# Performance work log

Hardware: AMD Instinct MI355X
Metric: run time of the kernel (lower is better)

The kernel has to match this reference:

```python
import jax, jax.numpy as jnp
import numpy as np

NG, NC, FG, FC, D = 8192, 4096, 512, 256, 64
ALPHA = 0.2          # leaky_relu negative slope
NEG = -9.0e15        # mask fill value from the torch code


def _leaky(x):
    return jnp.where(x >= 0, x, ALPHA * x)


def _relation(h_src, h_dst, a, adj):
    # additive GAT score: e[i,j] = leaky(h_src[i]@a[:D] + h_dst[j]@a[D:])
    s1 = h_src @ a[:D]            # [Ns]
    s2 = h_dst @ a[D:]            # [Nd]
    e = _leaky(s1[:, None] + s2[None, :])          # [Ns, Nd]
    att = jax.nn.softmax(jnp.where(adj > 0, e, NEG), axis=1)
    return att @ h_dst            # [Ns, D]


def setup_inputs() -> dict:
    key = jax.random.key(0)
    ks = jax.random.split(key, 14)
    sc = 0.05
    return {
        "gene_x": jax.random.normal(ks[0], (NG, FG), jnp.float32),
        "cell_x": jax.random.normal(ks[1], (NC, FC), jnp.float32),
        "W_g": jax.random.normal(ks[2], (FG, D), jnp.float32) * sc,
        "W_c": jax.random.normal(ks[3], (FC, D), jnp.float32) * sc,
        "a_gg": jax.random.normal(ks[4], (2 * D,), jnp.float32) * sc,
        "a_gc": jax.random.normal(ks[5], (2 * D,), jnp.float32) * sc,
        "a_cc": jax.random.normal(ks[6], (2 * D,), jnp.float32) * sc,
        "a_cg": jax.random.normal(ks[7], (2 * D,), jnp.float32) * sc,
        "Wgate_g": jax.random.normal(ks[8], (D, 1), jnp.float32) * sc,
        "bgate_g": jnp.full((1,), -2.0, jnp.float32),
        "Wgate_c": jax.random.normal(ks[9], (D, 1), jnp.float32) * sc,
        "bgate_c": jnp.full((1,), -2.0, jnp.float32),
        "gene_adj": jax.random.randint(ks[10], (NG, NG), 0, 2, jnp.int32),
        "cell_adj": jax.random.randint(ks[11], (NC, NC), 0, 2, jnp.int32),
        "gene_cell_adj": jax.random.randint(ks[12], (NG, NC), 0, 2, jnp.int32),
    }


def reference(gene_x, cell_x, W_g, W_c, a_gg, a_gc, a_cc, a_cg,
              Wgate_g, bgate_g, Wgate_c, bgate_c,
              gene_adj, cell_adj, gene_cell_adj):
    gene_h = gene_x @ W_g                              # [NG, D]
    cell_h = cell_x @ W_c                              # [NC, D]

    gene_from_gene = _relation(gene_h, gene_h, a_gg, gene_adj)
    gene_from_cell = _relation(gene_h, cell_h, a_gc, gene_cell_adj)
    cell_from_cell = _relation(cell_h, cell_h, a_cc, cell_adj)
    cell_from_gene = _relation(cell_h, gene_h, a_cg, gene_cell_adj.T)

    gamma_g = jax.nn.sigmoid(gene_h @ Wgate_g + bgate_g)   # [NG, 1]
    gamma_c = jax.nn.sigmoid(cell_h @ Wgate_c + bgate_c)   # [NC, 1]

    gene_out = _leaky(gene_h + gene_from_gene + gamma_g * gene_from_cell)
    cell_out = _leaky(cell_h + cell_from_cell + gamma_c * cell_from_gene)
    return gene_out, cell_out
```

## Files before the change

kernel.cpp:

```cpp
#include <hip/hip_runtime.h>

#define NG 8192
#define NC 4096
#define FG 512
#define FC 256
#define ALPHA 0.2f

typedef float f32x4 __attribute__((ext_vector_type(4)));
typedef short bf16x8 __attribute__((ext_vector_type(8)));

static __device__ __forceinline__ float leakyf(float x) { return fmaxf(x, ALPHA * x); }

static __device__ __forceinline__ unsigned short f2bf(float f) {
    unsigned u = __builtin_bit_cast(unsigned, f);
    u += 0x7fffu + ((u >> 16) & 1u);
    return (unsigned short)(u >> 16);
}

static __device__ __forceinline__ float wred(float v) {
#pragma unroll
    for (int m = 1; m < 64; m <<= 1) v += __shfl_xor(v, m, 64);
    return v;
}

__global__ __launch_bounds__(256) void proj_kernel(
    const float* __restrict__ x, const float* __restrict__ W, int K, int N,
    float* __restrict__ h, unsigned short* __restrict__ hT,
    const float* __restrict__ aA, const float* __restrict__ aB,
    const float* __restrict__ aC, const float* __restrict__ aD,
    const float* __restrict__ aG, const float* __restrict__ bG,
    float* __restrict__ sA, float* __restrict__ sB, float* __restrict__ sC,
    float* __restrict__ sD, float* __restrict__ gam)
{
    const int wave = threadIdx.x >> 6, lane = threadIdx.x & 63;
    const int r0 = blockIdx.x * 16 + wave * 4;
    const float* xr = x + (size_t)r0 * K;
    float acc0 = 0.f, acc1 = 0.f, acc2 = 0.f, acc3 = 0.f;
    for (int k = 0; k < K; k += 4) {
        float4 x0 = *(const float4*)(xr + k);
        float4 x1 = *(const float4*)(xr + K + k);
        float4 x2 = *(const float4*)(xr + 2 * (size_t)K + k);
        float4 x3 = *(const float4*)(xr + 3 * (size_t)K + k);
        float w0 = W[(k + 0) * 64 + lane];
        float w1 = W[(k + 1) * 64 + lane];
        float w2 = W[(k + 2) * 64 + lane];
        float w3 = W[(k + 3) * 64 + lane];
        acc0 += x0.x * w0 + x0.y * w1 + x0.z * w2 + x0.w * w3;
        acc1 += x1.x * w0 + x1.y * w1 + x1.z * w2 + x1.w * w3;
        acc2 += x2.x * w0 + x2.y * w1 + x2.z * w2 + x2.w * w3;
        acc3 += x3.x * w0 + x3.y * w1 + x3.z * w2 + x3.w * w3;
    }
    float accs[4] = {acc0, acc1, acc2, acc3};
    unsigned short hb[4];
#pragma unroll
    for (int t = 0; t < 4; t++) {
        h[(size_t)(r0 + t) * 64 + lane] = accs[t];
        hb[t] = f2bf(accs[t]);
    }
    *(ushort4*)&hT[(size_t)lane * N + r0] = make_ushort4(hb[0], hb[1], hb[2], hb[3]);

    const float cA = aA[lane], cB = aB[lane], cC = aC[lane], cD = aD[lane], cG = aG[lane];
    const float bias = bG[0];
#pragma unroll
    for (int t = 0; t < 4; t++) {
        float vA = wred(accs[t] * cA);
        float vB = wred(accs[t] * cB);
        float vC = wred(accs[t] * cC);
        float vD = wred(accs[t] * cD);
        float vG = wred(accs[t] * cG);
        if (lane == 0) {
            sA[r0 + t] = vA; sB[r0 + t] = vB; sC[r0 + t] = vC; sD[r0 + t] = vD;
            gam[r0 + t] = 1.f / (1.f + __expf(-(vG + bias)));
        }
    }
}

__global__ __launch_bounds__(256, 4) void rel_kernel(
    const int* __restrict__ adj, int adj_ld, int transposed,
    const float* __restrict__ s1, const float* __restrict__ s2,
    const unsigned short* __restrict__ hT, int Nd,
    float* __restrict__ num, float* __restrict__ lsum, int Ns, int JS)
{
    const int wave = threadIdx.x >> 6, lane = threadIdx.x & 63;
    const int m = lane & 15, kp = lane >> 4;
    const int strip = blockIdx.x, p = blockIdx.y;
    const int jlen = Nd / JS, jbase = p * jlen;
    const int i_row = strip * 64 + wave * 16 + m;
    const float s1v = s1[i_row];
    f32x4 acc0 = {0.f, 0.f, 0.f, 0.f}, acc1 = acc0, acc2 = acc0, acc3 = acc0;
    float lacc = 0.f;

    const unsigned short* hb0 = hT + (size_t)(0 * 16 + m) * Nd;
    const unsigned short* hb1 = hT + (size_t)(1 * 16 + m) * Nd;
    const unsigned short* hb2 = hT + (size_t)(2 * 16 + m) * Nd;
    const unsigned short* hb3 = hT + (size_t)(3 * 16 + m) * Nd;

    const int NGRP = jlen >> 5;
#pragma unroll 2
    for (int g = 0; g < NGRP; ++g) {
        const int jg = jbase + g * 32 + kp * 8;
        float4 sa = *(const float4*)&s2[jg];
        float4 sb = *(const float4*)&s2[jg + 4];
        int am[8];
        if (!transposed) {
            const int* ar = adj + (size_t)i_row * adj_ld + jg;
            int4 a0 = *(const int4*)ar;
            int4 a1 = *(const int4*)(ar + 4);
            am[0] = a0.x; am[1] = a0.y; am[2] = a0.z; am[3] = a0.w;
            am[4] = a1.x; am[5] = a1.y; am[6] = a1.z; am[7] = a1.w;
        } else {
            const int* ac = adj + (size_t)jg * adj_ld + i_row;
#pragma unroll
            for (int t = 0; t < 8; t++) am[t] = ac[(size_t)t * adj_ld];
        }
        bf16x8 b0 = *(const bf16x8*)&hb0[jg];
        bf16x8 b1 = *(const bf16x8*)&hb1[jg];
        bf16x8 b2 = *(const bf16x8*)&hb2[jg];
        bf16x8 b3 = *(const bf16x8*)&hb3[jg];

        float s2v[8] = {sa.x, sa.y, sa.z, sa.w, sb.x, sb.y, sb.z, sb.w};
        bf16x8 af;
#pragma unroll
        for (int t = 0; t < 8; t++) {
            float e = s1v + s2v[t];
            float w = (am[t] > 0) ? __expf(leakyf(e)) : 0.f;
            lacc += w;
            af[t] = (short)f2bf(w);
        }
        acc0 = __builtin_amdgcn_mfma_f32_16x16x32_bf16(af, b0, acc0, 0, 0, 0);
        acc1 = __builtin_amdgcn_mfma_f32_16x16x32_bf16(af, b1, acc1, 0, 0, 0);
        acc2 = __builtin_amdgcn_mfma_f32_16x16x32_bf16(af, b2, acc2, 0, 0, 0);
        acc3 = __builtin_amdgcn_mfma_f32_16x16x32_bf16(af, b3, acc3, 0, 0, 0);
    }
    const int orow0 = strip * 64 + wave * 16 + kp * 4;
#pragma unroll
    for (int r = 0; r < 4; r++) {
        size_t base = ((size_t)p * Ns + orow0 + r) * 64;
        num[base + m]      = acc0[r];
        num[base + 16 + m] = acc1[r];
        num[base + 32 + m] = acc2[r];
        num[base + 48 + m] = acc3[r];
    }
    lacc += __shfl_xor(lacc, 16, 64);
    lacc += __shfl_xor(lacc, 32, 64);
    if (kp == 0) lsum[(size_t)p * Ns + strip * 64 + wave * 16 + m] = lacc;
}

__global__ __launch_bounds__(256) void combine_final(
    const float* __restrict__ numS, const float* __restrict__ lS, int JSS,
    const float* __restrict__ numX, const float* __restrict__ lX, int JSX,
    int Ns, const float* __restrict__ h, const float* __restrict__ gam,
    float* __restrict__ out)
{
    int idx = blockIdx.x * 256 + threadIdx.x;
    int i = idx >> 6, c = idx & 63;
    float nS = 0.f, dS = 0.f, nX = 0.f, dX = 0.f;
    for (int p = 0; p < JSS; p++) {
        nS += numS[((size_t)p * Ns + i) * 64 + c];
        dS += lS[(size_t)p * Ns + i];
    }
    for (int p = 0; p < JSX; p++) {
        nX += numX[((size_t)p * Ns + i) * 64 + c];
        dX += lX[(size_t)p * Ns + i];
    }
    float v = h[idx] + nS / dS + gam[i] * (nX / dX);
    out[idx] = leakyf(v);
}

extern "C" void kernel_launch(void* const* d_in, const int* in_sizes, int n_in,
                              void* d_out, int out_size, void* d_ws, size_t ws_size,
                              hipStream_t stream)
{
    const float* gene_x = (const float*)d_in[0];
    const float* cell_x = (const float*)d_in[1];
    const float* W_g    = (const float*)d_in[2];
    const float* W_c    = (const float*)d_in[3];
    const float* a_gg   = (const float*)d_in[4];
    const float* a_gc   = (const float*)d_in[5];
    const float* a_cc   = (const float*)d_in[6];
    const float* a_cg   = (const float*)d_in[7];
    const float* Wgg    = (const float*)d_in[8];
    const float* bgg    = (const float*)d_in[9];
    const float* Wgc    = (const float*)d_in[10];
    const float* bgc    = (const float*)d_in[11];
    const int* gene_adj = (const int*)d_in[12];
    const int* cell_adj = (const int*)d_in[13];
    const int* gc_adj   = (const int*)d_in[14];

    size_t off = 0;
    char* wsb = (char*)d_ws;
    auto alloc = [&](size_t bytes) -> void* {
        void* p = wsb + off;
        off += (bytes + 255) & ~(size_t)255;
        return p;
    };
    const int JS_GG = 8, JS_CC = 16, JS_GC = 8, JS_CG = 16;

    float* gene_h = (float*)alloc((size_t)NG * 64 * 4);
    float* cell_h = (float*)alloc((size_t)NC * 64 * 4);
    unsigned short* gene_hT = (unsigned short*)alloc((size_t)NG * 64 * 2);
    unsigned short* cell_hT = (unsigned short*)alloc((size_t)NC * 64 * 2);
    float* s1gg = (float*)alloc(NG * 4);
    float* s2gg = (float*)alloc(NG * 4);
    float* s1gc = (float*)alloc(NG * 4);
    float* s2cg = (float*)alloc(NG * 4);
    float* gamg = (float*)alloc(NG * 4);
    float* s1cc = (float*)alloc(NC * 4);
    float* s2cc = (float*)alloc(NC * 4);
    float* s2gc = (float*)alloc(NC * 4);
    float* s1cg = (float*)alloc(NC * 4);
    float* gamc = (float*)alloc(NC * 4);
    float* numGG = (float*)alloc((size_t)NG * 64 * JS_GG * 4);
    float* lGG   = (float*)alloc((size_t)NG * JS_GG * 4);
    float* numGC = (float*)alloc((size_t)NG * 64 * JS_GC * 4);
    float* lGC   = (float*)alloc((size_t)NG * JS_GC * 4);
    float* numCC = (float*)alloc((size_t)NC * 64 * JS_CC * 4);
    float* lCC   = (float*)alloc((size_t)NC * JS_CC * 4);
    float* numCG = (float*)alloc((size_t)NC * 64 * JS_CG * 4);
    float* lCG   = (float*)alloc((size_t)NC * JS_CG * 4);

    float* out_gene = (float*)d_out;
    float* out_cell = (float*)d_out + (size_t)NG * 64;

    proj_kernel<<<NG / 16, 256, 0, stream>>>(gene_x, W_g, FG, NG, gene_h, gene_hT,
        a_gg, a_gg + 64, a_gc, a_cg + 64, Wgg, bgg, s1gg, s2gg, s1gc, s2cg, gamg);
    proj_kernel<<<NC / 16, 256, 0, stream>>>(cell_x, W_c, FC, NC, cell_h, cell_hT,
        a_cc, a_cc + 64, a_gc + 64, a_cg, Wgc, bgc, s1cc, s2cc, s2gc, s1cg, gamc);

    rel_kernel<<<dim3(NG / 64, JS_GG), 256, 0, stream>>>(gene_adj, NG, 0, s1gg, s2gg,
        gene_hT, NG, numGG, lGG, NG, JS_GG);
    rel_kernel<<<dim3(NC / 64, JS_CC), 256, 0, stream>>>(cell_adj, NC, 0, s1cc, s2cc,
        cell_hT, NC, numCC, lCC, NC, JS_CC);
    rel_kernel<<<dim3(NG / 64, JS_GC), 256, 0, stream>>>(gc_adj, NC, 0, s1gc, s2gc,
        cell_hT, NC, numGC, lGC, NG, JS_GC);
    rel_kernel<<<dim3(NC / 64, JS_CG), 256, 0, stream>>>(gc_adj, NC, 1, s1cg, s2cg,
        gene_hT, NG, numCG, lCG, NC, JS_CG);

    combine_final<<<NG * 64 / 256, 256, 0, stream>>>(numGG, lGG, JS_GG, numGC, lGC, JS_GC,
        NG, gene_h, gamg, out_gene);
    combine_final<<<NC * 64 / 256, 256, 0, stream>>>(numCC, lCC, JS_CC, numCG, lCG, JS_CG,
        NC, cell_h, gamc, out_cell);
}
```

Measured before the change: 763.0 us.

## Stage adjacency tiles into LDS with double-buffered async global_load_lds

Splits the relation kernel into row and column variants. Each wave stages its 16-row adjacency tile into LDS through double-buffered global_load_lds, waiting on vmcnt so the next chunk's loads overlap the current chunk's exp and MFMA work. The transposed case loads column tiles coalesced into a padded LDS layout. The J-split counts are cut, which means fewer partial sums to combine but also fewer blocks and lower occupancy, given the large LDS footprint and launch bounds of 1-2 blocks per CU.

```diff
diff --git a/kernel.cpp b/kernel.cpp
--- a/kernel.cpp
+++ b/kernel.cpp
@@ -8,6 +8,9 @@
 
 typedef float f32x4 __attribute__((ext_vector_type(4)));
 typedef short bf16x8 __attribute__((ext_vector_type(8)));
+
+#define AS1C(p) ((const __attribute__((address_space(1))) void*)(p))
+#define AS3(p)  ((__attribute__((address_space(3))) void*)(p))
 
 static __device__ __forceinline__ float leakyf(float x) { return fmaxf(x, ALPHA * x); }
 
@@ -75,62 +78,170 @@
     }
 }
 
-__global__ __launch_bounds__(256, 4) void rel_kernel(
-    const int* __restrict__ adj, int adj_ld, int transposed,
+__global__ __launch_bounds__(256, 1) void rel_row(
+    const int* __restrict__ adj, int adj_ld,
     const float* __restrict__ s1, const float* __restrict__ s2,
     const unsigned short* __restrict__ hT, int Nd,
     float* __restrict__ num, float* __restrict__ lsum, int Ns, int JS)
 {
+    __shared__ int smem[4 * 2 * 16 * 260];
     const int wave = threadIdx.x >> 6, lane = threadIdx.x & 63;
     const int m = lane & 15, kp = lane >> 4;
     const int strip = blockIdx.x, p = blockIdx.y;
     const int jlen = Nd / JS, jbase = p * jlen;
-    const int i_row = strip * 64 + wave * 16 + m;
-    const float s1v = s1[i_row];
-    f32x4 acc0 = {0.f, 0.f, 0.f, 0.f}, acc1 = acc0, acc2 = acc0, acc3 = acc0;
-    float lacc = 0.f;
+    const int i0w = strip * 64 + wave * 16;
+    const float s1v = s1[i0w + m];
+    int* wbuf = smem + wave * (2 * 16 * 260);
+    const int* arow = adj + (size_t)i0w * adj_ld + jbase;
 
     const unsigned short* hb0 = hT + (size_t)(0 * 16 + m) * Nd;
     const unsigned short* hb1 = hT + (size_t)(1 * 16 + m) * Nd;
     const unsigned short* hb2 = hT + (size_t)(2 * 16 + m) * Nd;
     const unsigned short* hb3 = hT + (size_t)(3 * 16 + m) * Nd;
 
-    const int NGRP = jlen >> 5;
-#pragma unroll 2
-    for (int g = 0; g < NGRP; ++g) {
-        const int jg = jbase + g * 32 + kp * 8;
-        float4 sa = *(const float4*)&s2[jg];
-        float4 sb = *(const float4*)&s2[jg + 4];
-        int am[8];
-        if (!transposed) {
-            const int* ar = adj + (size_t)i_row * adj_ld + jg;
-            int4 a0 = *(const int4*)ar;
-            int4 a1 = *(const int4*)(ar + 4);
-            am[0] = a0.x; am[1] = a0.y; am[2] = a0.z; am[3] = a0.w;
-            am[4] = a1.x; am[5] = a1.y; am[6] = a1.z; am[7] = a1.w;
+    f32x4 acc0 = {0.f, 0.f, 0.f, 0.f}, acc1 = acc0, acc2 = acc0, acc3 = acc0;
+    float lacc = 0.f;
+    const int NCH = jlen >> 8;
+
+    {
+        int* dst = wbuf;
+#pragma unroll
+        for (int r = 0; r < 16; ++r)
+            __builtin_amdgcn_global_load_lds(AS1C(arow + (size_t)r * adj_ld + lane * 4),
+                                             AS3(dst + r * 260), 16, 0, 0);
+    }
+    for (int c = 0; c < NCH; ++c) {
+        int* cur = wbuf + (c & 1) * (16 * 260);
+        if (c + 1 < NCH) {
+            int* dst = wbuf + ((c + 1) & 1) * (16 * 260);
+            const int* src = arow + (c + 1) * 256;
+#pragma unroll
+            for (int r = 0; r < 16; ++r)
+                __builtin_amdgcn_global_load_lds(AS1C(src + (size_t)r * adj_ld + lane * 4),
+                                                 AS3(dst + r * 260), 16, 0, 0);
+            asm volatile("s_waitcnt vmcnt(16)" ::: "memory");
         } else {
-            const int* ac = adj + (size_t)jg * adj_ld + i_row;
-#pragma unroll
-            for (int t = 0; t < 8; t++) am[t] = ac[(size_t)t * adj_ld];
-        }
-        bf16x8 b0 = *(const bf16x8*)&hb0[jg];
-        bf16x8 b1 = *(const bf16x8*)&hb1[jg];
-        bf16x8 b2 = *(const bf16x8*)&hb2[jg];
-        bf16x8 b3 = *(const bf16x8*)&hb3[jg];
-
-        float s2v[8] = {sa.x, sa.y, sa.z, sa.w, sb.x, sb.y, sb.z, sb.w};
-        bf16x8 af;
-#pragma unroll
-        for (int t = 0; t < 8; t++) {
-            float e = s1v + s2v[t];
-            float w = (am[t] > 0) ? __expf(leakyf(e)) : 0.f;
-            lacc += w;
-            af[t] = (short)f2bf(w);
-        }
-        acc0 = __builtin_amdgcn_mfma_f32_16x16x32_bf16(af, b0, acc0, 0, 0, 0);
-        acc1 = __builtin_amdgcn_mfma_f32_16x16x32_bf16(af, b1, acc1, 0, 0, 0);
-        acc2 = __builtin_amdgcn_mfma_f32_16x16x32_bf16(af, b2, acc2, 0, 0, 0);
-        acc3 = __builtin_amdgcn_mfma_f32_16x16x32_bf16(af, b3, acc3, 0, 0, 0);
+            asm volatile("s_waitcnt vmcnt(0)" ::: "memory");
+        }
+        const int jc = jbase + c * 256;
+#pragma unroll
+        for (int g = 0; g < 8; ++g) {
+            const int jg = jc + g * 32 + kp * 8;
+            float4 sa = *(const float4*)&s2[jg];
+            float4 sb = *(const float4*)&s2[jg + 4];
+            const int* ap = cur + m * 260 + g * 32 + kp * 8;
+            int4 a0 = *(const int4*)ap;
+            int4 a1 = *(const int4*)(ap + 4);
+            bf16x8 b0 = *(const bf16x8*)&hb0[jg];
+            bf16x8 b1 = *(const bf16x8*)&hb1[jg];
+            bf16x8 b2 = *(const bf16x8*)&hb2[jg];
+            bf16x8 b3 = *(const bf16x8*)&hb3[jg];
+            float s2v[8] = {sa.x, sa.y, sa.z, sa.w, sb.x, sb.y, sb.z, sb.w};
+            int am[8] = {a0.x, a0.y, a0.z, a0.w, a1.x, a1.y, a1.z, a1.w};
+            bf16x8 af;
+#pragma unroll
+            for (int t = 0; t < 8; t++) {
+                float e = s1v + s2v[t];
+                float w = (am[t] > 0) ? __expf(leakyf(e)) : 0.f;
+                lacc += w;
+                af[t] = (short)f2bf(w);
+            }
+            acc0 = __builtin_amdgcn_mfma_f32_16x16x32_bf16(af, b0, acc0, 0, 0, 0);
+            acc1 = __builtin_amdgcn_mfma_f32_16x16x32_bf16(af, b1, acc1, 0, 0, 0);
+            acc2 = __builtin_amdgcn_mfma_f32_16x16x32_bf16(af, b2, acc2, 0, 0, 0);
+            acc3 = __builtin_amdgcn_mfma_f32_16x16x32_bf16(af, b3, acc3, 0, 0, 0);
+        }
+    }
+    const int orow0 = strip * 64 + wave * 16 + kp * 4;
+#pragma unroll
+    for (int r = 0; r < 4; r++) {
+        size_t base = ((size_t)p * Ns + orow0 + r) * 64;
+        num[base + m]      = acc0[r];
+        num[base + 16 + m] = acc1[r];
+        num[base + 32 + m] = acc2[r];
+        num[base + 48 + m] = acc3[r];
+    }
+    lacc += __shfl_xor(lacc, 16, 64);
+    lacc += __shfl_xor(lacc, 32, 64);
+    if (kp == 0) lsum[(size_t)p * Ns + strip * 64 + wave * 16 + m] = lacc;
+}
+
+__global__ __launch_bounds__(256, 2) void rel_col(
+    const int* __restrict__ adj, int adj_ld,
+    const float* __restrict__ s1, const float* __restrict__ s2,
+    const unsigned short* __restrict__ hT, int Nd,
+    float* __restrict__ num, float* __restrict__ lsum, int Ns, int JS)
+{
+    __shared__ int smem[4 * 2 * 32 * 68];
+    const int wave = threadIdx.x >> 6, lane = threadIdx.x & 63;
+    const int m = lane & 15, kp = lane >> 4;
+    const int strip = blockIdx.x, p = blockIdx.y;
+    const int jlen = Nd / JS, jbase = p * jlen;
+    const int i0w = strip * 64 + wave * 16;
+    const float s1v = s1[i0w + m];
+    int* wbuf = smem + wave * (2 * 32 * 68);
+    const int lr = lane >> 4, li = lane & 15;
+
+    const unsigned short* hb0 = hT + (size_t)(0 * 16 + m) * Nd;
+    const unsigned short* hb1 = hT + (size_t)(1 * 16 + m) * Nd;
+    const unsigned short* hb2 = hT + (size_t)(2 * 16 + m) * Nd;
+    const unsigned short* hb3 = hT + (size_t)(3 * 16 + m) * Nd;
+
+    f32x4 acc0 = {0.f, 0.f, 0.f, 0.f}, acc1 = acc0, acc2 = acc0, acc3 = acc0;
+    float lacc = 0.f;
+    const int NCH = jlen >> 7;
+
+    {
+        int* dst = wbuf;
+#pragma unroll
+        for (int q = 0; q < 32; ++q)
+            __builtin_amdgcn_global_load_lds(
+                AS1C(adj + (size_t)(jbase + q * 4 + lr) * adj_ld + i0w + li),
+                AS3(dst + q * 68), 4, 0, 0);
+    }
+    for (int c = 0; c < NCH; ++c) {
+        int* cur = wbuf + (c & 1) * (32 * 68);
+        if (c + 1 < NCH) {
+            int* dst = wbuf + ((c + 1) & 1) * (32 * 68);
+            const int jn = jbase + (c + 1) * 128;
+#pragma unroll
+            for (int q = 0; q < 32; ++q)
+                __builtin_amdgcn_global_load_lds(
+                    AS1C(adj + (size_t)(jn + q * 4 + lr) * adj_ld + i0w + li),
+                    AS3(dst + q * 68), 4, 0, 0);
+            asm volatile("s_waitcnt vmcnt(32)" ::: "memory");
+        } else {
+            asm volatile("s_waitcnt vmcnt(0)" ::: "memory");
+        }
+        const int jc = jbase + c * 128;
+#pragma unroll
+        for (int g = 0; g < 4; ++g) {
+            const int jg = jc + g * 32 + kp * 8;
+            float4 sa = *(const float4*)&s2[jg];
+            float4 sb = *(const float4*)&s2[jg + 4];
+            const int* ap = cur + (g * 8 + kp * 2) * 68 + m;
+            int am[8];
+#pragma unroll
+            for (int t = 0; t < 8; t++)
+                am[t] = ap[(t >> 2) * 68 + (t & 3) * 16];
+            bf16x8 b0 = *(const bf16x8*)&hb0[jg];
+            bf16x8 b1 = *(const bf16x8*)&hb1[jg];
+            bf16x8 b2 = *(const bf16x8*)&hb2[jg];
+            bf16x8 b3 = *(const bf16x8*)&hb3[jg];
+            float s2v[8] = {sa.x, sa.y, sa.z, sa.w, sb.x, sb.y, sb.z, sb.w};
+            bf16x8 af;
+#pragma unroll
+            for (int t = 0; t < 8; t++) {
+                float e = s1v + s2v[t];
+                float w = (am[t] > 0) ? __expf(leakyf(e)) : 0.f;
+                lacc += w;
+                af[t] = (short)f2bf(w);
+            }
+            acc0 = __builtin_amdgcn_mfma_f32_16x16x32_bf16(af, b0, acc0, 0, 0, 0);
+            acc1 = __builtin_amdgcn_mfma_f32_16x16x32_bf16(af, b1, acc1, 0, 0, 0);
+            acc2 = __builtin_amdgcn_mfma_f32_16x16x32_bf16(af, b2, acc2, 0, 0, 0);
+            acc3 = __builtin_amdgcn_mfma_f32_16x16x32_bf16(af, b3, acc3, 0, 0, 0);
+        }
     }
     const int orow0 = strip * 64 + wave * 16 + kp * 4;
 #pragma unroll
@@ -194,7 +305,7 @@
         off += (bytes + 255) & ~(size_t)255;
         return p;
     };
-    const int JS_GG = 8, JS_CC = 16, JS_GC = 8, JS_CG = 16;
+    const int JS_GG = 2, JS_CC = 4, JS_GC = 2, JS_CG = 8;
 
     float* gene_h = (float*)alloc((size_t)NG * 64 * 4);
     float* cell_h = (float*)alloc((size_t)NC * 64 * 4);
@@ -227,13 +338,13 @@
     proj_kernel<<<NC / 16, 256, 0, stream>>>(cell_x, W_c, FC, NC, cell_h, cell_hT,
         a_cc, a_cc + 64, a_gc + 64, a_cg, Wgc, bgc, s1cc, s2cc, s2gc, s1cg, gamc);
 
-    rel_kernel<<<dim3(NG / 64, JS_GG), 256, 0, stream>>>(gene_adj, NG, 0, s1gg, s2gg,
+    rel_row<<<dim3(NG / 64, JS_GG), 256, 0, stream>>>(gene_adj, NG, s1gg, s2gg,
         gene_hT, NG, numGG, lGG, NG, JS_GG);
-    rel_kernel<<<dim3(NC / 64, JS_CC), 256, 0, stream>>>(cell_adj, NC, 0, s1cc, s2cc,
+    rel_row<<<dim3(NC / 64, JS_CC), 256, 0, stream>>>(cell_adj, NC, s1cc, s2cc,
         cell_hT, NC, numCC, lCC, NC, JS_CC);
-    rel_kernel<<<dim3(NG / 64, JS_GC), 256, 0, stream>>>(gc_adj, NC, 0, s1gc, s2gc,
+    rel_row<<<dim3(NG / 64, JS_GC), 256, 0, stream>>>(gc_adj, NC, s1gc, s2gc,
         cell_hT, NC, numGC, lGC, NG, JS_GC);
-    rel_kernel<<<dim3(NC / 64, JS_CG), 256, 0, stream>>>(gc_adj, NC, 1, s1cg, s2cg,
+    rel_col<<<dim3(NC / 64, JS_CG), 256, 0, stream>>>(gc_adj, NC, s1cg, s2cg,
         gene_hT, NG, numCG, lCG, NC, JS_CG);
 
     combine_final<<<NG * 64 / 256, 256, 0, stream>>>(numGG, lGG, JS_GG, numGC, lGC, JS_GC,
```

New measurement: 772.0 us. No clear change (+1.2%).

## Pack adjacency into bitmasks once and stage hT tiles in LDS

Applied to the files above, without the earlier changes.

Adds a pack_bits pass that turns each int32 adjacency matrix into a bitmask, so the four relation kernels read a compact mask rather than full ints. The shared gene-cell mask also serves the transposed relation. The relation kernel is split into row and column variants that stage hT tiles (and mask bytes for the column case) in shared memory. The split factors JS are halved. The int adjacency must still be read once in full, so the gain depends on the gene-cell matrix being reused and on cheaper transposed access, at the cost of extra launches, LDS traffic and barriers.

```diff
diff --git a/kernel.cpp b/kernel.cpp
--- a/kernel.cpp
+++ b/kernel.cpp
@@ -21,6 +21,24 @@
 #pragma unroll
     for (int m = 1; m < 64; m <<= 1) v += __shfl_xor(v, m, 64);
     return v;
+}
+
+__global__ __launch_bounds__(256) void pack_bits(
+    const int* __restrict__ adj, int C, unsigned char* __restrict__ bm)
+{
+    const int wave = threadIdx.x >> 6, lane = threadIdx.x & 63;
+    const int r = blockIdx.x * 4 + wave;
+    const int* row = adj + (size_t)r * C;
+    unsigned char* brow = bm + (size_t)r * (C >> 3);
+    for (int j = lane * 8; j < C; j += 512) {
+        int4 a0 = *(const int4*)(row + j);
+        int4 a1 = *(const int4*)(row + j + 4);
+        unsigned b = (unsigned)(a0.x > 0)        | ((unsigned)(a0.y > 0) << 1)
+                   | ((unsigned)(a0.z > 0) << 2) | ((unsigned)(a0.w > 0) << 3)
+                   | ((unsigned)(a1.x > 0) << 4) | ((unsigned)(a1.y > 0) << 5)
+                   | ((unsigned)(a1.z > 0) << 6) | ((unsigned)(a1.w > 0) << 7);
+        brow[j >> 3] = (unsigned char)b;
+    }
 }
 
 __global__ __launch_bounds__(256) void proj_kernel(
@@ -75,62 +93,128 @@
     }
 }
 
-__global__ __launch_bounds__(256, 4) void rel_kernel(
-    const int* __restrict__ adj, int adj_ld, int transposed,
+__global__ __launch_bounds__(256, 4) void rel_row(
+    const unsigned char* __restrict__ bm, int bm_ld,
     const float* __restrict__ s1, const float* __restrict__ s2,
     const unsigned short* __restrict__ hT, int Nd,
     float* __restrict__ num, float* __restrict__ lsum, int Ns, int JS)
 {
+    __shared__ unsigned short hbuf[64 * 264];
     const int wave = threadIdx.x >> 6, lane = threadIdx.x & 63;
     const int m = lane & 15, kp = lane >> 4;
     const int strip = blockIdx.x, p = blockIdx.y;
     const int jlen = Nd / JS, jbase = p * jlen;
     const int i_row = strip * 64 + wave * 16 + m;
     const float s1v = s1[i_row];
+    const unsigned char* bmrow = bm + (size_t)i_row * bm_ld;
     f32x4 acc0 = {0.f, 0.f, 0.f, 0.f}, acc1 = acc0, acc2 = acc0, acc3 = acc0;
     float lacc = 0.f;
 
-    const unsigned short* hb0 = hT + (size_t)(0 * 16 + m) * Nd;
-    const unsigned short* hb1 = hT + (size_t)(1 * 16 + m) * Nd;
-    const unsigned short* hb2 = hT + (size_t)(2 * 16 + m) * Nd;
-    const unsigned short* hb3 = hT + (size_t)(3 * 16 + m) * Nd;
-
-    const int NGRP = jlen >> 5;
-#pragma unroll 2
-    for (int g = 0; g < NGRP; ++g) {
-        const int jg = jbase + g * 32 + kp * 8;
-        float4 sa = *(const float4*)&s2[jg];
-        float4 sb = *(const float4*)&s2[jg + 4];
-        int am[8];
-        if (!transposed) {
-            const int* ar = adj + (size_t)i_row * adj_ld + jg;
-            int4 a0 = *(const int4*)ar;
-            int4 a1 = *(const int4*)(ar + 4);
-            am[0] = a0.x; am[1] = a0.y; am[2] = a0.z; am[3] = a0.w;
-            am[4] = a1.x; am[5] = a1.y; am[6] = a1.z; am[7] = a1.w;
-        } else {
-            const int* ac = adj + (size_t)jg * adj_ld + i_row;
-#pragma unroll
-            for (int t = 0; t < 8; t++) am[t] = ac[(size_t)t * adj_ld];
-        }
-        bf16x8 b0 = *(const bf16x8*)&hb0[jg];
-        bf16x8 b1 = *(const bf16x8*)&hb1[jg];
-        bf16x8 b2 = *(const bf16x8*)&hb2[jg];
-        bf16x8 b3 = *(const bf16x8*)&hb3[jg];
-
-        float s2v[8] = {sa.x, sa.y, sa.z, sa.w, sb.x, sb.y, sb.z, sb.w};
-        bf16x8 af;
-#pragma unroll
-        for (int t = 0; t < 8; t++) {
-            float e = s1v + s2v[t];
-            float w = (am[t] > 0) ? __expf(leakyf(e)) : 0.f;
-            lacc += w;
-            af[t] = (short)f2bf(w);
-        }
-        acc0 = __builtin_amdgcn_mfma_f32_16x16x32_bf16(af, b0, acc0, 0, 0, 0);
-        acc1 = __builtin_amdgcn_mfma_f32_16x16x32_bf16(af, b1, acc1, 0, 0, 0);
-        acc2 = __builtin_amdgcn_mfma_f32_16x16x32_bf16(af, b2, acc2, 0, 0, 0);
-        acc3 = __builtin_amdgcn_mfma_f32_16x16x32_bf16(af, b3, acc3, 0, 0, 0);
+    for (int jc = jbase; jc < jbase + jlen; jc += 256) {
+        uint4 q0 = *(const uint4*)(bmrow + (jc >> 3));
+        uint4 q1 = *(const uint4*)(bmrow + (jc >> 3) + 16);
+        for (int idx = threadIdx.x; idx < 2048; idx += 256) {
+            int c = idx >> 5, off = (idx & 31) * 8;
+            *(int4*)&hbuf[c * 264 + off] = *(const int4*)&hT[(size_t)c * Nd + jc + off];
+        }
+        __syncthreads();
+        unsigned words[8] = {q0.x, q0.y, q0.z, q0.w, q1.x, q1.y, q1.z, q1.w};
+#pragma unroll
+        for (int g = 0; g < 8; ++g) {
+            const int jg = jc + g * 32 + kp * 8;
+            float4 sa = *(const float4*)&s2[jg];
+            float4 sb = *(const float4*)&s2[jg + 4];
+            unsigned byte = (words[g] >> (kp * 8)) & 0xffu;
+            const int lb = g * 32 + kp * 8;
+            bf16x8 b0 = *(const bf16x8*)&hbuf[(0 * 16 + m) * 264 + lb];
+            bf16x8 b1 = *(const bf16x8*)&hbuf[(1 * 16 + m) * 264 + lb];
+            bf16x8 b2 = *(const bf16x8*)&hbuf[(2 * 16 + m) * 264 + lb];
+            bf16x8 b3 = *(const bf16x8*)&hbuf[(3 * 16 + m) * 264 + lb];
+            float s2v[8] = {sa.x, sa.y, sa.z, sa.w, sb.x, sb.y, sb.z, sb.w};
+            bf16x8 af;
+#pragma unroll
+            for (int t = 0; t < 8; t++) {
+                float e = s1v + s2v[t];
+                float w = ((byte >> t) & 1u) ? __expf(leakyf(e)) : 0.f;
+                lacc += w;
+                af[t] = (short)f2bf(w);
+            }
+            acc0 = __builtin_amdgcn_mfma_f32_16x16x32_bf16(af, b0, acc0, 0, 0, 0);
+            acc1 = __builtin_amdgcn_mfma_f32_16x16x32_bf16(af, b1, acc1, 0, 0, 0);
+            acc2 = __builtin_amdgcn_mfma_f32_16x16x32_bf16(af, b2, acc2, 0, 0, 0);
+            acc3 = __builtin_amdgcn_mfma_f32_16x16x32_bf16(af, b3, acc3, 0, 0, 0);
+        }
+        __syncthreads();
+    }
+    const int orow0 = strip * 64 + wave * 16 + kp * 4;
+#pragma unroll
+    for (int r = 0; r < 4; r++) {
+        size_t base = ((size_t)p * Ns + orow0 + r) * 64;
+        num[base + m]      = acc0[r];
+        num[base + 16 + m] = acc1[r];
+        num[base + 32 + m] = acc2[r];
+        num[base + 48 + m] = acc3[r];
+    }
+    lacc += __shfl_xor(lacc, 16, 64);
+    lacc += __shfl_xor(lacc, 32, 64);
+    if (kp == 0) lsum[(size_t)p * Ns + strip * 64 + wave * 16 + m] = lacc;
+}
+
+__global__ __launch_bounds__(256, 4) void rel_col(
+    const unsigned char* __restrict__ bm, int bm_ld,
+    const float* __restrict__ s1, const float* __restrict__ s2,
+    const unsigned short* __restrict__ hT, int Nd,
+    float* __restrict__ num, float* __restrict__ lsum, int Ns, int JS)
+{
+    __shared__ unsigned short hbuf[64 * 136];
+    __shared__ unsigned char bmb[128 * 8];
+    const int wave = threadIdx.x >> 6, lane = threadIdx.x & 63;
+    const int m = lane & 15, kp = lane >> 4;
+    const int strip = blockIdx.x, p = blockIdx.y;
+    const int jlen = Nd / JS, jbase = p * jlen;
+    const int i0 = strip * 64;
+    const float s1v = s1[i0 + wave * 16 + m];
+    f32x4 acc0 = {0.f, 0.f, 0.f, 0.f}, acc1 = acc0, acc2 = acc0, acc3 = acc0;
+    float lacc = 0.f;
+    const int bidx = wave * 2 + (m >> 3);
+    const int bbit = m & 7;
+
+    for (int jc = jbase; jc < jbase + jlen; jc += 128) {
+        if (threadIdx.x < 128)
+            *(unsigned long long*)&bmb[threadIdx.x * 8] =
+                *(const unsigned long long*)&bm[(size_t)(jc + threadIdx.x) * bm_ld + (i0 >> 3)];
+        for (int idx = threadIdx.x; idx < 1024; idx += 256) {
+            int c = idx >> 4, off = (idx & 15) * 8;
+            *(int4*)&hbuf[c * 136 + off] = *(const int4*)&hT[(size_t)c * Nd + jc + off];
+        }
+        __syncthreads();
+#pragma unroll
+        for (int g = 0; g < 4; ++g) {
+            const int jg = jc + g * 32 + kp * 8;
+            float4 sa = *(const float4*)&s2[jg];
+            float4 sb = *(const float4*)&s2[jg + 4];
+            const int jl = g * 32 + kp * 8;
+            const int lb = jl;
+            bf16x8 b0 = *(const bf16x8*)&hbuf[(0 * 16 + m) * 136 + lb];
+            bf16x8 b1 = *(const bf16x8*)&hbuf[(1 * 16 + m) * 136 + lb];
+            bf16x8 b2 = *(const bf16x8*)&hbuf[(2 * 16 + m) * 136 + lb];
+            bf16x8 b3 = *(const bf16x8*)&hbuf[(3 * 16 + m) * 136 + lb];
+            float s2v[8] = {sa.x, sa.y, sa.z, sa.w, sb.x, sb.y, sb.z, sb.w};
+            bf16x8 af;
+#pragma unroll
+            for (int t = 0; t < 8; t++) {
+                unsigned byte = bmb[(jl + t) * 8 + bidx];
+                float e = s1v + s2v[t];
+                float w = ((byte >> bbit) & 1u) ? __expf(leakyf(e)) : 0.f;
+                lacc += w;
+                af[t] = (short)f2bf(w);
+            }
+            acc0 = __builtin_amdgcn_mfma_f32_16x16x32_bf16(af, b0, acc0, 0, 0, 0);
+            acc1 = __builtin_amdgcn_mfma_f32_16x16x32_bf16(af, b1, acc1, 0, 0, 0);
+            acc2 = __builtin_amdgcn_mfma_f32_16x16x32_bf16(af, b2, acc2, 0, 0, 0);
+            acc3 = __builtin_amdgcn_mfma_f32_16x16x32_bf16(af, b3, acc3, 0, 0, 0);
+        }
+        __syncthreads();
     }
     const int orow0 = strip * 64 + wave * 16 + kp * 4;
 #pragma unroll
@@ -194,12 +278,15 @@
         off += (bytes + 255) & ~(size_t)255;
         return p;
     };
-    const int JS_GG = 8, JS_CC = 16, JS_GC = 8, JS_CG = 16;
+    const int JS_GG = 4, JS_CC = 8, JS_GC = 4, JS_CG = 8;
 
     float* gene_h = (float*)alloc((size_t)NG * 64 * 4);
     float* cell_h = (float*)alloc((size_t)NC * 64 * 4);
     unsigned short* gene_hT = (unsigned short*)alloc((size_t)NG * 64 * 2);
     unsigned short* cell_hT = (unsigned short*)alloc((size_t)NC * 64 * 2);
+    unsigned char* bmGG = (unsigned char*)alloc((size_t)NG * (NG / 8));
+    unsigned char* bmCC = (unsigned char*)alloc((size_t)NC * (NC / 8));
+    unsigned char* bmGC = (unsigned char*)alloc((size_t)NG * (NC / 8));
     float* s1gg = (float*)alloc(NG * 4);
     float* s2gg = (float*)alloc(NG * 4);
     float* s1gc = (float*)alloc(NG * 4);
@@ -222,18 +309,22 @@
     float* out_gene = (float*)d_out;
     float* out_cell = (float*)d_out + (size_t)NG * 64;
 
+    pack_bits<<<NG / 4, 256, 0, stream>>>(gene_adj, NG, bmGG);
+    pack_bits<<<NC / 4, 256, 0, stream>>>(cell_adj, NC, bmCC);
+    pack_bits<<<NG / 4, 256, 0, stream>>>(gc_adj, NC, bmGC);
+
     proj_kernel<<<NG / 16, 256, 0, stream>>>(gene_x, W_g, FG, NG, gene_h, gene_hT,
         a_gg, a_gg + 64, a_gc, a_cg + 64, Wgg, bgg, s1gg, s2gg, s1gc, s2cg, gamg);
     proj_kernel<<<NC / 16, 256, 0, stream>>>(cell_x, W_c, FC, NC, cell_h, cell_hT,
         a_cc, a_cc + 64, a_gc + 64, a_cg, Wgc, bgc, s1cc, s2cc, s2gc, s1cg, gamc);
 
-    rel_kernel<<<dim3(NG / 64, JS_GG), 256, 0, stream>>>(gene_adj, NG, 0, s1gg, s2gg,
+    rel_row<<<dim3(NG / 64, JS_GG), 256, 0, stream>>>(bmGG, NG / 8, s1gg, s2gg,
         gene_hT, NG, numGG, lGG, NG, JS_GG);
-    rel_kernel<<<dim3(NC / 64, JS_CC), 256, 0, stream>>>(cell_adj, NC, 0, s1cc, s2cc,
+    rel_row<<<dim3(NC / 64, JS_CC), 256, 0, stream>>>(bmCC, NC / 8, s1cc, s2cc,
         cell_hT, NC, numCC, lCC, NC, JS_CC);
-    rel_kernel<<<dim3(NG / 64, JS_GC), 256, 0, stream>>>(gc_adj, NC, 0, s1gc, s2gc,
+    rel_row<<<dim3(NG / 64, JS_GC), 256, 0, stream>>>(bmGC, NC / 8, s1gc, s2gc,
         cell_hT, NC, numGC, lGC, NG, JS_GC);
-    rel_kernel<<<dim3(NC / 64, JS_CG), 256, 0, stream>>>(gc_adj, NC, 1, s1cg, s2cg,
+    rel_col<<<dim3(NC / 64, JS_CG), 256, 0, stream>>>(bmGC, NC / 8, s1cg, s2cg,
         gene_hT, NG, numCG, lCG, NC, JS_CG);
 
     combine_final<<<NG * 64 / 256, 256, 0, stream>>>(numGG, lGG, JS_GG, numGC, lGC, JS_GC,
```

New measurement: 765.0 us. No clear change (+0.3%).
